# Performance work log

Measured on AMD Instinct MI355X. Metric: run time of the kernel, lower is better.

## Reference

```python
import jax, jax.numpy as jnp
import numpy as np

MARGIN = 0.1
N_SUBSETS = 3
NEG_INF = -1e30


def setup_inputs() -> dict:
    key = jax.random.key(0)
    k1, k2 = jax.random.split(key)
    B, D = 12288, 128
    emb = jax.random.normal(k1, (B, D), dtype=jnp.float32)
    emb = emb / jnp.linalg.norm(emb, axis=-1, keepdims=True)  # cosine-style sims in [-1,1]
    target = jax.random.randint(k2, (B,), 0, 512, dtype=jnp.int64)
    return {"emb": emb, "target": target}


def _subset_loss(e, t):
    # e: [m, D], t: [m]
    m = e.shape[0]
    sim = e @ e.T                                   # [m, m]
    same = t[:, None] == t[None, :]
    eye = jnp.eye(m, dtype=bool)
    pos = same & ~eye                                # positives, diagonal excluded
    neg = ~same                                      # negatives (diag is 'same', so excluded)
    max_neg = jnp.max(jnp.where(neg, sim, NEG_INF), axis=1)   # neg_pair_[-1]
    max_pos = jnp.max(jnp.where(pos, sim, NEG_INF), axis=1)   # pos_pair_[-1]
    # select pos sims < max_neg + margin; loss = sum(1 - pos)
    pos_sel = pos & (sim < (max_neg + MARGIN)[:, None])
    pos_loss = jnp.sum(jnp.where(pos_sel, 1.0 - sim, 0.0), axis=1)
    # select neg sims > max(0.6, max_pos) - margin; loss = sum(neg)
    thr = jnp.maximum(jnp.float32(0.6), max_pos) - MARGIN
    neg_sel = neg & (sim > thr[:, None])
    neg_loss = jnp.sum(jnp.where(neg_sel, sim, 0.0), axis=1)
    has_pos = jnp.any(pos, axis=1)
    row_loss = jnp.where(has_pos, pos_loss + neg_loss, 0.0)
    return jnp.mean(row_loss)  # sum(loss)/n


def reference(emb, target):
    B, D = emb.shape
    m = B // N_SUBSETS
    e = emb.reshape(N_SUBSETS, m, D)
    t = target.reshape(N_SUBSETS, m)
    losses = jax.vmap(_subset_loss)(e, t)  # [n_subsets]
    return jnp.mean(losses)
```

## Files before the change

kernel.cpp:

```cpp
#include <hip/hip_runtime.h>
#include <stdint.h>

typedef __bf16 bf16x8 __attribute__((ext_vector_type(8)));
typedef float f32x4 __attribute__((ext_vector_type(4)));
typedef unsigned short ushort8v __attribute__((ext_vector_type(8)));

static constexpr int SUBSETS = 3;
static constexpr int M = 4096;
static constexpr int D = 128;

static constexpr int WG_ROWS = 128;
static constexpr int WG_COLS = 256;
static constexpr int NSTRIP = M / WG_COLS;
static constexpr int NRBWG = M / WG_ROWS;
static constexpr int WGS = SUBSETS * NRBWG * NSTRIP;
static constexpr int SCOLS = 32;
static constexpr int NSTAGE = WG_COLS / SCOLS;

#define MARGIN_F 0.1f
#define NEGINF (-1e30f)

__global__ void cvt_f32_bf16(const float* __restrict__ in,
                             unsigned short* __restrict__ out, int n8,
                             float* __restrict__ loss_out) {
    int i = blockIdx.x * blockDim.x + threadIdx.x;
    if (i == 0) *loss_out = 0.0f;
    if (i >= n8) return;
    const float4* p = reinterpret_cast<const float4*>(in) + (size_t)i * 2;
    float4 a = p[0];
    float4 b = p[1];
    float v[8] = {a.x, a.y, a.z, a.w, b.x, b.y, b.z, b.w};
    ushort8v r;
#pragma unroll
    for (int j = 0; j < 8; ++j) {
        uint32_t u = __builtin_bit_cast(uint32_t, v[j]);
        u = (u + 0x7FFFu + ((u >> 16) & 1u)) >> 16;
        r[j] = (unsigned short)u;
    }
    *(reinterpret_cast<ushort8v*>(out) + i) = r;
}

__device__ __forceinline__ void stage_tile(const unsigned short* __restrict__ base,
                                           unsigned short* __restrict__ ldsbuf,
                                           int w, int lane) {
#pragma unroll
    for (int i = 0; i < 2; ++i) {
        const int slocal = w * 2048 + i * 1024 + lane * 16;
        const int col = slocal >> 8;
        const int off = (slocal & 255) ^ ((col & 7) << 4);
        const char* gsrc = (const char*)base + col * 256 + off;
        char* ldst = (char*)ldsbuf + w * 2048 + i * 1024;
        __builtin_amdgcn_global_load_lds(
            (const __attribute__((address_space(1))) void*)gsrc,
            (__attribute__((address_space(3))) void*)ldst,
            16, 0, 0);
    }
}

__device__ __forceinline__ bf16x8 lds_bfrag(const unsigned short* __restrict__ ldsbuf,
                                            int tt, int llo, int lhi, int kb) {
    const int col = tt * 16 + llo;
    const int off = (kb * 64 + lhi * 16) ^ ((col & 7) << 4);
    return *reinterpret_cast<const bf16x8*>((const char*)ldsbuf + col * 256 + off);
}

__global__ __launch_bounds__(256) void pass_max(
        const unsigned short* __restrict__ ebf,
        const int* __restrict__ tgt,
        float* __restrict__ wsmax) {
    __shared__ unsigned short lds[2][SCOLS * D];

    const int wg = blockIdx.x;
    const int s = wg >> 9;
    const int rem = wg & 511;
    const int rbWG = rem & 31;
    const int cs = rem >> 5;

    const int tid = threadIdx.x;
    const int w = tid >> 6, lane = tid & 63;
    const int lhi = lane >> 4, llo = lane & 15;

    const unsigned short* E = ebf + (size_t)s * M * D;
    const int* T = tgt + s * M;
    const int rowBase = rbWG * WG_ROWS + w * 32;
    const int colBase = cs * WG_COLS;

    stage_tile(E + (size_t)colBase * D, lds[0], w, lane);

    bf16x8 a[2][4];
#pragma unroll
    for (int rr = 0; rr < 2; ++rr) {
        const int row = rowBase + rr * 16 + llo;
#pragma unroll
        for (int kb = 0; kb < 4; ++kb)
            a[rr][kb] = *reinterpret_cast<const bf16x8*>(
                E + (size_t)row * D + kb * 32 + lhi * 8);
    }
    int trow[2][4];
#pragma unroll
    for (int rr = 0; rr < 2; ++rr)
#pragma unroll
        for (int r = 0; r < 4; ++r)
            trow[rr][r] = T[rowBase + rr * 16 + lhi * 4 + r];

    float mp[2][4], mn[2][4];
#pragma unroll
    for (int rr = 0; rr < 2; ++rr)
#pragma unroll
        for (int r = 0; r < 4; ++r) { mp[rr][r] = NEGINF; mn[rr][r] = NEGINF; }

    __syncthreads();

    for (int st = 0; st < NSTAGE; ++st) {
        const int buf = st & 1;
        if (st + 1 < NSTAGE)
            stage_tile(E + (size_t)(colBase + (st + 1) * SCOLS) * D, lds[buf ^ 1], w, lane);
#pragma unroll
        for (int tt = 0; tt < 2; ++tt) {
            const int bcol = colBase + st * SCOLS + tt * 16 + llo;
            bf16x8 b[4];
#pragma unroll
            for (int kb = 0; kb < 4; ++kb) b[kb] = lds_bfrag(lds[buf], tt, llo, lhi, kb);
            const int tcol = T[bcol];
#pragma unroll
            for (int rr = 0; rr < 2; ++rr) {
                f32x4 acc = {0.f, 0.f, 0.f, 0.f};
#pragma unroll
                for (int kb = 0; kb < 4; ++kb)
                    acc = __builtin_amdgcn_mfma_f32_16x16x32_bf16(a[rr][kb], b[kb], acc, 0, 0, 0);
#pragma unroll
                for (int r = 0; r < 4; ++r) {
                    const float sv = acc[r];
                    const int rowG = rowBase + rr * 16 + lhi * 4 + r;
                    if (tcol == trow[rr][r]) {
                        if (rowG != bcol) mp[rr][r] = fmaxf(mp[rr][r], sv);
                    } else {
                        mn[rr][r] = fmaxf(mn[rr][r], sv);
                    }
                }
            }
        }
        __syncthreads();
    }

#pragma unroll
    for (int rr = 0; rr < 2; ++rr)
#pragma unroll
        for (int r = 0; r < 4; ++r) {
#pragma unroll
            for (int off = 1; off < 16; off <<= 1) {
                mp[rr][r] = fmaxf(mp[rr][r], __shfl_xor(mp[rr][r], off));
                mn[rr][r] = fmaxf(mn[rr][r], __shfl_xor(mn[rr][r], off));
            }
        }
    if (llo == 0) {
#pragma unroll
        for (int rr = 0; rr < 2; ++rr)
#pragma unroll
            for (int r = 0; r < 4; ++r) {
                const int row = rowBase + rr * 16 + lhi * 4 + r;
                wsmax[((size_t)(0 * SUBSETS + s) * M + row) * NSTRIP + cs] = mp[rr][r];
                wsmax[((size_t)(1 * SUBSETS + s) * M + row) * NSTRIP + cs] = mn[rr][r];
            }
    }
}

__global__ __launch_bounds__(256) void pass_sum(
        const unsigned short* __restrict__ ebf,
        const int* __restrict__ tgt,
        const float* __restrict__ wsmax,
        float* __restrict__ out) {
    __shared__ unsigned short lds[2][SCOLS * D];
    __shared__ float wsum[4];

    const int wg = blockIdx.x;
    const int s = wg >> 9;
    const int rem = wg & 511;
    const int rbWG = rem & 31;
    const int cs = rem >> 5;

    const int tid = threadIdx.x;
    const int w = tid >> 6, lane = tid & 63;
    const int lhi = lane >> 4, llo = lane & 15;

    const unsigned short* E = ebf + (size_t)s * M * D;
    const int* T = tgt + s * M;
    const int rowBase = rbWG * WG_ROWS + w * 32;
    const int colBase = cs * WG_COLS;

    stage_tile(E + (size_t)colBase * D, lds[0], w, lane);

    float thrP[2][4], thrN[2][4], hasPos[2][4];
#pragma unroll
    for (int rr = 0; rr < 2; ++rr)
#pragma unroll
        for (int r = 0; r < 4; ++r) {
            const int row = rowBase + rr * 16 + lhi * 4 + r;
            float vp = wsmax[((size_t)(0 * SUBSETS + s) * M + row) * NSTRIP + llo];
            float vn = wsmax[((size_t)(1 * SUBSETS + s) * M + row) * NSTRIP + llo];
#pragma unroll
            for (int off = 1; off < 16; off <<= 1) {
                vp = fmaxf(vp, __shfl_xor(vp, off));
                vn = fmaxf(vn, __shfl_xor(vn, off));
            }
            thrP[rr][r] = vn + MARGIN_F;
            thrN[rr][r] = fmaxf(0.6f, vp) - MARGIN_F;
            hasPos[rr][r] = (vp > -1e29f) ? 1.0f : 0.0f;
        }

    bf16x8 a[2][4];
#pragma unroll
    for (int rr = 0; rr < 2; ++rr) {
        const int row = rowBase + rr * 16 + llo;
#pragma unroll
        for (int kb = 0; kb < 4; ++kb)
            a[rr][kb] = *reinterpret_cast<const bf16x8*>(
                E + (size_t)row * D + kb * 32 + lhi * 8);
    }
    int trow[2][4];
#pragma unroll
    for (int rr = 0; rr < 2; ++rr)
#pragma unroll
        for (int r = 0; r < 4; ++r)
            trow[rr][r] = T[rowBase + rr * 16 + lhi * 4 + r];

    float acl[2][4] = {{0.f, 0.f, 0.f, 0.f}, {0.f, 0.f, 0.f, 0.f}};

    __syncthreads();

    for (int st = 0; st < NSTAGE; ++st) {
        const int buf = st & 1;
        if (st + 1 < NSTAGE)
            stage_tile(E + (size_t)(colBase + (st + 1) * SCOLS) * D, lds[buf ^ 1], w, lane);
#pragma unroll
        for (int tt = 0; tt < 2; ++tt) {
            const int bcol = colBase + st * SCOLS + tt * 16 + llo;
            bf16x8 b[4];
#pragma unroll
            for (int kb = 0; kb < 4; ++kb) b[kb] = lds_bfrag(lds[buf], tt, llo, lhi, kb);
            const int tcol = T[bcol];
#pragma unroll
            for (int rr = 0; rr < 2; ++rr) {
                f32x4 acc = {0.f, 0.f, 0.f, 0.f};
#pragma unroll
                for (int kb = 0; kb < 4; ++kb)
                    acc = __builtin_amdgcn_mfma_f32_16x16x32_bf16(a[rr][kb], b[kb], acc, 0, 0, 0);
#pragma unroll
                for (int r = 0; r < 4; ++r) {
                    const float sv = acc[r];
                    const int rowG = rowBase + rr * 16 + lhi * 4 + r;
                    if (tcol == trow[rr][r]) {
                        if (rowG != bcol && sv < thrP[rr][r]) acl[rr][r] += 1.0f - sv;
                    } else {
                        if (sv > thrN[rr][r]) acl[rr][r] += sv;
                    }
                }
            }
        }
        __syncthreads();
    }

    float tot = 0.f;
#pragma unroll
    for (int rr = 0; rr < 2; ++rr)
#pragma unroll
        for (int r = 0; r < 4; ++r) tot += acl[rr][r] * hasPos[rr][r];
#pragma unroll
    for (int off = 1; off < 64; off <<= 1) tot += __shfl_xor(tot, off);

    if (lane == 0) wsum[w] = tot;
    __syncthreads();
    if (tid == 0)
        atomicAdd(out, (wsum[0] + wsum[1] + wsum[2] + wsum[3]) * (1.0f / 12288.0f));
}

extern "C" void kernel_launch(void* const* d_in, const int* in_sizes, int n_in,
                              void* d_out, int out_size, void* d_ws, size_t ws_size,
                              hipStream_t stream) {
    const float* emb = (const float*)d_in[0];
    const int* tgt = (const int*)d_in[1];
    float* out = (float*)d_out;

    unsigned short* ebf = (unsigned short*)d_ws;
    float* wsmax = (float*)((char*)d_ws + (size_t)SUBSETS * M * D * 2);

    const int n = SUBSETS * M * D;
    const int n8 = n / 8;

    cvt_f32_bf16<<<n8 / 256, 256, 0, stream>>>(emb, ebf, n8, out);
    pass_max<<<WGS, 256, 0, stream>>>(ebf, tgt, wsmax);
    pass_sum<<<WGS, 256, 0, stream>>>(ebf, tgt, wsmax, out);
}
```

Measured before the change: 130.3 us.

## Double row-panel height per workgroup and make epilogue branchless

Each workgroup now covers 256 rows instead of 128, so each wave holds four 16-row A fragments and reuses every staged B tile from LDS for twice as many MFMAs. This halves the workgroup count and the redundant B-tile staging. The per-element masking in both passes becomes branchless selects instead of divergent if/else. The hasPos multiply is folded into the thresholds (NEGINF/POSINF), so it no longer needs extra registers. The larger per-wave register footprint may reduce occupancy, and fewer workgroups may leave compute units underused.

```diff
diff --git a/kernel.cpp b/kernel.cpp
--- a/kernel.cpp
+++ b/kernel.cpp
@@ -9,16 +9,17 @@
 static constexpr int M = 4096;
 static constexpr int D = 128;
 
-static constexpr int WG_ROWS = 128;
+static constexpr int WG_ROWS = 256;
 static constexpr int WG_COLS = 256;
 static constexpr int NSTRIP = M / WG_COLS;
-static constexpr int NRBWG = M / WG_ROWS;
-static constexpr int WGS = SUBSETS * NRBWG * NSTRIP;
+static constexpr int NPANEL = M / WG_ROWS;
+static constexpr int WGS = SUBSETS * NPANEL * NSTRIP;
 static constexpr int SCOLS = 32;
 static constexpr int NSTAGE = WG_COLS / SCOLS;
 
 #define MARGIN_F 0.1f
 #define NEGINF (-1e30f)
+#define POSINF (1e30f)
 
 __global__ void cvt_f32_bf16(const float* __restrict__ in,
                              unsigned short* __restrict__ out, int n8,
@@ -71,10 +72,10 @@
     __shared__ unsigned short lds[2][SCOLS * D];
 
     const int wg = blockIdx.x;
-    const int s = wg >> 9;
-    const int rem = wg & 511;
-    const int rbWG = rem & 31;
-    const int cs = rem >> 5;
+    const int s = wg >> 8;
+    const int rem = wg & 255;
+    const int panel = rem & (NPANEL - 1);
+    const int cs = rem >> 4;
 
     const int tid = threadIdx.x;
     const int w = tid >> 6, lane = tid & 63;
@@ -82,30 +83,30 @@
 
     const unsigned short* E = ebf + (size_t)s * M * D;
     const int* T = tgt + s * M;
-    const int rowBase = rbWG * WG_ROWS + w * 32;
+    const int rowBase = panel * WG_ROWS + w * 64;
     const int colBase = cs * WG_COLS;
 
     stage_tile(E + (size_t)colBase * D, lds[0], w, lane);
 
-    bf16x8 a[2][4];
-#pragma unroll
-    for (int rr = 0; rr < 2; ++rr) {
+    bf16x8 a[4][4];
+#pragma unroll
+    for (int rr = 0; rr < 4; ++rr) {
         const int row = rowBase + rr * 16 + llo;
 #pragma unroll
         for (int kb = 0; kb < 4; ++kb)
             a[rr][kb] = *reinterpret_cast<const bf16x8*>(
                 E + (size_t)row * D + kb * 32 + lhi * 8);
     }
-    int trow[2][4];
-#pragma unroll
-    for (int rr = 0; rr < 2; ++rr)
+    int trow[4][4];
+#pragma unroll
+    for (int rr = 0; rr < 4; ++rr)
 #pragma unroll
         for (int r = 0; r < 4; ++r)
             trow[rr][r] = T[rowBase + rr * 16 + lhi * 4 + r];
 
-    float mp[2][4], mn[2][4];
-#pragma unroll
-    for (int rr = 0; rr < 2; ++rr)
+    float mp[4][4], mn[4][4];
+#pragma unroll
+    for (int rr = 0; rr < 4; ++rr)
 #pragma unroll
         for (int r = 0; r < 4; ++r) { mp[rr][r] = NEGINF; mn[rr][r] = NEGINF; }
 
@@ -123,7 +124,7 @@
             for (int kb = 0; kb < 4; ++kb) b[kb] = lds_bfrag(lds[buf], tt, llo, lhi, kb);
             const int tcol = T[bcol];
 #pragma unroll
-            for (int rr = 0; rr < 2; ++rr) {
+            for (int rr = 0; rr < 4; ++rr) {
                 f32x4 acc = {0.f, 0.f, 0.f, 0.f};
 #pragma unroll
                 for (int kb = 0; kb < 4; ++kb)
@@ -132,11 +133,10 @@
                 for (int r = 0; r < 4; ++r) {
                     const float sv = acc[r];
                     const int rowG = rowBase + rr * 16 + lhi * 4 + r;
-                    if (tcol == trow[rr][r]) {
-                        if (rowG != bcol) mp[rr][r] = fmaxf(mp[rr][r], sv);
-                    } else {
-                        mn[rr][r] = fmaxf(mn[rr][r], sv);
-                    }
+                    const bool same = (tcol == trow[rr][r]);
+                    const bool offd = (rowG != bcol);
+                    mp[rr][r] = fmaxf(mp[rr][r], (same && offd) ? sv : NEGINF);
+                    mn[rr][r] = fmaxf(mn[rr][r], same ? NEGINF : sv);
                 }
             }
         }
@@ -144,7 +144,7 @@
     }
 
 #pragma unroll
-    for (int rr = 0; rr < 2; ++rr)
+    for (int rr = 0; rr < 4; ++rr)
 #pragma unroll
         for (int r = 0; r < 4; ++r) {
 #pragma unroll
@@ -155,7 +155,7 @@
         }
     if (llo == 0) {
 #pragma unroll
-        for (int rr = 0; rr < 2; ++rr)
+        for (int rr = 0; rr < 4; ++rr)
 #pragma unroll
             for (int r = 0; r < 4; ++r) {
                 const int row = rowBase + rr * 16 + lhi * 4 + r;
@@ -174,10 +174,10 @@
     __shared__ float wsum[4];
 
     const int wg = blockIdx.x;
-    const int s = wg >> 9;
-    const int rem = wg & 511;
-    const int rbWG = rem & 31;
-    const int cs = rem >> 5;
+    const int s = wg >> 8;
+    const int rem = wg & 255;
+    const int panel = rem & (NPANEL - 1);
+    const int cs = rem >> 4;
 
     const int tid = threadIdx.x;
     const int w = tid >> 6, lane = tid & 63;
@@ -185,14 +185,14 @@
 
     const unsigned short* E = ebf + (size_t)s * M * D;
     const int* T = tgt + s * M;
-    const int rowBase = rbWG * WG_ROWS + w * 32;
+    const int rowBase = panel * WG_ROWS + w * 64;
     const int colBase = cs * WG_COLS;
 
     stage_tile(E + (size_t)colBase * D, lds[0], w, lane);
 
-    float thrP[2][4], thrN[2][4], hasPos[2][4];
-#pragma unroll
-    for (int rr = 0; rr < 2; ++rr)
+    float thrP[4][4], thrN[4][4];
+#pragma unroll
+    for (int rr = 0; rr < 4; ++rr)
 #pragma unroll
         for (int r = 0; r < 4; ++r) {
             const int row = rowBase + rr * 16 + lhi * 4 + r;
@@ -203,28 +203,32 @@
                 vp = fmaxf(vp, __shfl_xor(vp, off));
                 vn = fmaxf(vn, __shfl_xor(vn, off));
             }
-            thrP[rr][r] = vn + MARGIN_F;
-            thrN[rr][r] = fmaxf(0.6f, vp) - MARGIN_F;
-            hasPos[rr][r] = (vp > -1e29f) ? 1.0f : 0.0f;
-        }
-
-    bf16x8 a[2][4];
-#pragma unroll
-    for (int rr = 0; rr < 2; ++rr) {
+            const bool hasPos = (vp > -1e29f);
+            thrP[rr][r] = hasPos ? vn + MARGIN_F : NEGINF;
+            thrN[rr][r] = hasPos ? fmaxf(0.6f, vp) - MARGIN_F : POSINF;
+        }
+
+    bf16x8 a[4][4];
+#pragma unroll
+    for (int rr = 0; rr < 4; ++rr) {
         const int row = rowBase + rr * 16 + llo;
 #pragma unroll
         for (int kb = 0; kb < 4; ++kb)
             a[rr][kb] = *reinterpret_cast<const bf16x8*>(
                 E + (size_t)row * D + kb * 32 + lhi * 8);
     }
-    int trow[2][4];
-#pragma unroll
-    for (int rr = 0; rr < 2; ++rr)
+    int trow[4][4];
+#pragma unroll
+    for (int rr = 0; rr < 4; ++rr)
 #pragma unroll
         for (int r = 0; r < 4; ++r)
             trow[rr][r] = T[rowBase + rr * 16 + lhi * 4 + r];
 
-    float acl[2][4] = {{0.f, 0.f, 0.f, 0.f}, {0.f, 0.f, 0.f, 0.f}};
+    float acl[4][4];
+#pragma unroll
+    for (int rr = 0; rr < 4; ++rr)
+#pragma unroll
+        for (int r = 0; r < 4; ++r) acl[rr][r] = 0.f;
 
     __syncthreads();
 
@@ -240,7 +244,7 @@
             for (int kb = 0; kb < 4; ++kb) b[kb] = lds_bfrag(lds[buf], tt, llo, lhi, kb);
             const int tcol = T[bcol];
 #pragma unroll
-            for (int rr = 0; rr < 2; ++rr) {
+            for (int rr = 0; rr < 4; ++rr) {
                 f32x4 acc = {0.f, 0.f, 0.f, 0.f};
 #pragma unroll
                 for (int kb = 0; kb < 4; ++kb)
@@ -249,11 +253,11 @@
                 for (int r = 0; r < 4; ++r) {
                     const float sv = acc[r];
                     const int rowG = rowBase + rr * 16 + lhi * 4 + r;
-                    if (tcol == trow[rr][r]) {
-                        if (rowG != bcol && sv < thrP[rr][r]) acl[rr][r] += 1.0f - sv;
-                    } else {
-                        if (sv > thrN[rr][r]) acl[rr][r] += sv;
-                    }
+                    const bool same = (tcol == trow[rr][r]);
+                    const bool offd = (rowG != bcol);
+                    const float addp = (same && offd && (sv < thrP[rr][r])) ? (1.0f - sv) : 0.0f;
+                    const float addn = (!same && (sv > thrN[rr][r])) ? sv : 0.0f;
+                    acl[rr][r] += addp + addn;
                 }
             }
         }
@@ -262,9 +266,9 @@
 
     float tot = 0.f;
 #pragma unroll
-    for (int rr = 0; rr < 2; ++rr)
-#pragma unroll
-        for (int r = 0; r < 4; ++r) tot += acl[rr][r] * hasPos[rr][r];
+    for (int rr = 0; rr < 4; ++rr)
+#pragma unroll
+        for (int r = 0; r < 4; ++r) tot += acl[rr][r];
 #pragma unroll
     for (int off = 1; off < 64; off <<= 1) tot += __shfl_xor(tot, off);
 
```

Result: faster. 126.2 us (-3.2%).

## Store bf16 similarity matrix in first pass, select from it instead of recomputing GEMM

Applied to the files above, without the earlier changes.

The max pass now also writes every similarity tile to workspace as packed bf16 (about 100MB total). A new pass_sel kernel streams those tiles back to apply the thresholds, so the second GEMM is not recomputed. The original recompute path is kept as a fallback when the workspace is too small. The branches in both passes are also rewritten as branchless selects. This trades MFMA recompute for a large extra global write and read, and selecting on bf16-rounded sims can change which borderline pairs pass the thresholds.

```diff
diff --git a/kernel.cpp b/kernel.cpp
--- a/kernel.cpp
+++ b/kernel.cpp
@@ -8,17 +8,23 @@
 static constexpr int SUBSETS = 3;
 static constexpr int M = 4096;
 static constexpr int D = 128;
+static constexpr int MT = M / 16;
 
 static constexpr int WG_ROWS = 128;
 static constexpr int WG_COLS = 256;
 static constexpr int NSTRIP = M / WG_COLS;
 static constexpr int NRBWG = M / WG_ROWS;
-static constexpr int WGS = SUBSETS * NRBWG * NSTRIP;
+static constexpr int WGS1 = SUBSETS * NRBWG * NSTRIP;
 static constexpr int SCOLS = 32;
 static constexpr int NSTAGE = WG_COLS / SCOLS;
 
+static constexpr int SEL_NCS = 4;
+static constexpr int SEL_WAVES = SUBSETS * MT * SEL_NCS;
+static constexpr int WGS2 = SEL_WAVES / 4;
+
 #define MARGIN_F 0.1f
 #define NEGINF (-1e30f)
+#define POSINF (1e30f)
 
 __global__ void cvt_f32_bf16(const float* __restrict__ in,
                              unsigned short* __restrict__ out, int n8,
@@ -64,10 +70,12 @@
     return *reinterpret_cast<const bf16x8*>((const char*)ldsbuf + col * 256 + off);
 }
 
-__global__ __launch_bounds__(256) void pass_max(
+template <int STORE>
+__global__ __launch_bounds__(256) void pass_gemm(
         const unsigned short* __restrict__ ebf,
         const int* __restrict__ tgt,
-        float* __restrict__ wsmax) {
+        float* __restrict__ wsmax,
+        char* __restrict__ sims) {
     __shared__ unsigned short lds[2][SCOLS * D];
 
     const int wg = blockIdx.x;
@@ -84,6 +92,7 @@
     const int* T = tgt + s * M;
     const int rowBase = rbWG * WG_ROWS + w * 32;
     const int colBase = cs * WG_COLS;
+    const int rt0 = rowBase >> 4;
 
     stage_tile(E + (size_t)colBase * D, lds[0], w, lane);
 
@@ -118,6 +127,7 @@
 #pragma unroll
         for (int tt = 0; tt < 2; ++tt) {
             const int bcol = colBase + st * SCOLS + tt * 16 + llo;
+            const int ct = (colBase + st * SCOLS + tt * 16) >> 4;
             bf16x8 b[4];
 #pragma unroll
             for (int kb = 0; kb < 4; ++kb) b[kb] = lds_bfrag(lds[buf], tt, llo, lhi, kb);
@@ -132,11 +142,19 @@
                 for (int r = 0; r < 4; ++r) {
                     const float sv = acc[r];
                     const int rowG = rowBase + rr * 16 + lhi * 4 + r;
-                    if (tcol == trow[rr][r]) {
-                        if (rowG != bcol) mp[rr][r] = fmaxf(mp[rr][r], sv);
-                    } else {
-                        mn[rr][r] = fmaxf(mn[rr][r], sv);
-                    }
+                    const bool same = (tcol == trow[rr][r]);
+                    const bool offd = (rowG != bcol);
+                    mp[rr][r] = fmaxf(mp[rr][r], (same && offd) ? sv : NEGINF);
+                    mn[rr][r] = fmaxf(mn[rr][r], same ? NEGINF : sv);
+                }
+                if (STORE) {
+                    uint32_t p0, p1;
+                    asm("v_cvt_pk_bf16_f32 %0, %1, %2" : "=v"(p0) : "v"(acc[0]), "v"(acc[1]));
+                    asm("v_cvt_pk_bf16_f32 %0, %1, %2" : "=v"(p1) : "v"(acc[2]), "v"(acc[3]));
+                    char* tb = sims + (((size_t)(s * MT + rt0 + rr) * MT + ct) << 9)
+                                    + llo * 32 + lhi * 8;
+                    uint2 pv; pv.x = p0; pv.y = p1;
+                    *reinterpret_cast<uint2*>(tb) = pv;
                 }
             }
         }
@@ -165,7 +183,82 @@
     }
 }
 
-__global__ __launch_bounds__(256) void pass_sum(
+__global__ __launch_bounds__(256) void pass_sel(
+        const char* __restrict__ sims,
+        const int* __restrict__ tgt,
+        const float* __restrict__ wsmax,
+        float* __restrict__ out) {
+    const int gwid = blockIdx.x * 4 + (threadIdx.x >> 6);
+    const int lane = threadIdx.x & 63;
+    const int s = gwid >> 10;
+    const int rem = gwid & 1023;
+    const int rt = rem & (MT - 1);
+    const int csel = rem >> 8;
+    const int lhi = lane >> 4, llo = lane & 15;
+
+    const int* T = tgt + s * M;
+    const int rowBase = rt * 16;
+
+    float thrP[4], thrN[4];
+#pragma unroll
+    for (int r = 0; r < 4; ++r) {
+        const int row = rowBase + lhi * 4 + r;
+        float vp = wsmax[((size_t)(0 * SUBSETS + s) * M + row) * NSTRIP + llo];
+        float vn = wsmax[((size_t)(1 * SUBSETS + s) * M + row) * NSTRIP + llo];
+#pragma unroll
+        for (int off = 1; off < 16; off <<= 1) {
+            vp = fmaxf(vp, __shfl_xor(vp, off));
+            vn = fmaxf(vn, __shfl_xor(vn, off));
+        }
+        const bool hasPos = (vp > -1e29f);
+        thrP[r] = hasPos ? vn + MARGIN_F : NEGINF;
+        thrN[r] = hasPos ? fmaxf(0.6f, vp) - MARGIN_F : POSINF;
+    }
+    int trow[4];
+#pragma unroll
+    for (int r = 0; r < 4; ++r) trow[r] = T[rowBase + lhi * 4 + r];
+
+    const char* base = sims + (((size_t)(s * MT + rt) * MT) << 9) + llo * 32 + lhi * 8;
+    const int ct0 = csel * 64;
+
+    float tot = 0.f;
+    auto proc = [&](uint2 dv, int tcol, int ct) {
+        const int colG = ct * 16 + llo;
+        uint32_t bits[4] = {dv.x << 16, dv.x & 0xffff0000u,
+                            dv.y << 16, dv.y & 0xffff0000u};
+#pragma unroll
+        for (int r = 0; r < 4; ++r) {
+            const float sv = __builtin_bit_cast(float, bits[r]);
+            const int rowG = rowBase + lhi * 4 + r;
+            const bool same = (tcol == trow[r]);
+            const bool offd = (rowG != colG);
+            const float addp = (same && offd && (sv < thrP[r])) ? (1.0f - sv) : 0.0f;
+            const float addn = (!same && (sv > thrN[r])) ? sv : 0.0f;
+            tot += addp + addn;
+        }
+    };
+
+    uint2 dA, dB;
+    int tcA, tcB;
+    dA = *reinterpret_cast<const uint2*>(base + ((size_t)ct0 << 9));
+    tcA = T[ct0 * 16 + llo];
+#pragma unroll 2
+    for (int t = 0; t < 64; ++t) {
+        const int ct = ct0 + t;
+        if (t + 1 < 64) {
+            dB = *reinterpret_cast<const uint2*>(base + ((size_t)(ct + 1) << 9));
+            tcB = T[(ct + 1) * 16 + llo];
+        }
+        proc(dA, tcA, ct);
+        dA = dB; tcA = tcB;
+    }
+
+#pragma unroll
+    for (int off = 1; off < 64; off <<= 1) tot += __shfl_xor(tot, off);
+    if (lane == 0) atomicAdd(out, tot * (1.0f / 12288.0f));
+}
+
+__global__ __launch_bounds__(256) void pass_sum_fb(
         const unsigned short* __restrict__ ebf,
         const int* __restrict__ tgt,
         const float* __restrict__ wsmax,
@@ -190,7 +283,7 @@
 
     stage_tile(E + (size_t)colBase * D, lds[0], w, lane);
 
-    float thrP[2][4], thrN[2][4], hasPos[2][4];
+    float thrP[2][4], thrN[2][4];
 #pragma unroll
     for (int rr = 0; rr < 2; ++rr)
 #pragma unroll
@@ -203,9 +296,9 @@
                 vp = fmaxf(vp, __shfl_xor(vp, off));
                 vn = fmaxf(vn, __shfl_xor(vn, off));
             }
-            thrP[rr][r] = vn + MARGIN_F;
-            thrN[rr][r] = fmaxf(0.6f, vp) - MARGIN_F;
-            hasPos[rr][r] = (vp > -1e29f) ? 1.0f : 0.0f;
+            const bool hasPos = (vp > -1e29f);
+            thrP[rr][r] = hasPos ? vn + MARGIN_F : NEGINF;
+            thrN[rr][r] = hasPos ? fmaxf(0.6f, vp) - MARGIN_F : POSINF;
         }
 
     bf16x8 a[2][4];
@@ -224,8 +317,7 @@
         for (int r = 0; r < 4; ++r)
             trow[rr][r] = T[rowBase + rr * 16 + lhi * 4 + r];
 
-    float acl[2][4] = {{0.f, 0.f, 0.f, 0.f}, {0.f, 0.f, 0.f, 0.f}};
-
+    float acl = 0.f;
     __syncthreads();
 
     for (int st = 0; st < NSTAGE; ++st) {
@@ -249,25 +341,20 @@
                 for (int r = 0; r < 4; ++r) {
                     const float sv = acc[r];
                     const int rowG = rowBase + rr * 16 + lhi * 4 + r;
-                    if (tcol == trow[rr][r]) {
-                        if (rowG != bcol && sv < thrP[rr][r]) acl[rr][r] += 1.0f - sv;
-                    } else {
-                        if (sv > thrN[rr][r]) acl[rr][r] += sv;
-                    }
+                    const bool same = (tcol == trow[rr][r]);
+                    const bool offd = (rowG != bcol);
+                    const float addp = (same && offd && (sv < thrP[rr][r])) ? (1.0f - sv) : 0.0f;
+                    const float addn = (!same && (sv > thrN[rr][r])) ? sv : 0.0f;
+                    acl += addp + addn;
                 }
             }
         }
         __syncthreads();
     }
 
-    float tot = 0.f;
-#pragma unroll
-    for (int rr = 0; rr < 2; ++rr)
-#pragma unroll
-        for (int r = 0; r < 4; ++r) tot += acl[rr][r] * hasPos[rr][r];
+    float tot = acl;
 #pragma unroll
     for (int off = 1; off < 64; off <<= 1) tot += __shfl_xor(tot, off);
-
     if (lane == 0) wsum[w] = tot;
     __syncthreads();
     if (tid == 0)
@@ -283,11 +370,19 @@
 
     unsigned short* ebf = (unsigned short*)d_ws;
     float* wsmax = (float*)((char*)d_ws + (size_t)SUBSETS * M * D * 2);
+    char* sims = (char*)d_ws + (8u << 20);
+
+    const size_t need = (8u << 20) + (size_t)SUBSETS * M * M * 2;
 
     const int n = SUBSETS * M * D;
     const int n8 = n / 8;
 
     cvt_f32_bf16<<<n8 / 256, 256, 0, stream>>>(emb, ebf, n8, out);
-    pass_max<<<WGS, 256, 0, stream>>>(ebf, tgt, wsmax);
-    pass_sum<<<WGS, 256, 0, stream>>>(ebf, tgt, wsmax, out);
-}
+    if (ws_size >= need) {
+        pass_gemm<1><<<WGS1, 256, 0, stream>>>(ebf, tgt, wsmax, sims);
+        pass_sel<<<WGS2, 256, 0, stream>>>(sims, tgt, wsmax, out);
+    } else {
+        pass_gemm<0><<<WGS1, 256, 0, stream>>>(ebf, tgt, wsmax, sims);
+        pass_sum_fb<<<WGS1, 256, 0, stream>>>(ebf, tgt, wsmax, out);
+    }
+}
```

Measured after the change: 149.4 us. +14.7%, slower.
